# Kernel tuning notes

Hardware: AMD Instinct MI355X
Metric: run time of the kernel (lower is better)

Reference implementation:

```python
import jax, jax.numpy as jnp
import numpy as np

N_BASIS = 8
CUTOFF = 5.0
NORM_FACTOR = 16.0


def setup_inputs() -> dict:
    key = jax.random.key(0)
    ks = jax.random.split(key, 10)
    N, E, C = 20000, 320000, 32
    s = 1.0 / np.sqrt(C)
    return {
        "node0": jax.random.normal(ks[0], (N, C), jnp.float32),
        "node1": jax.random.normal(ks[1], (N, C, 3), jnp.float32),
        "node2": jax.random.normal(ks[2], (N, C, 3, 3), jnp.float32),
        "rij": jax.random.normal(ks[3], (E, 3), jnp.float32) * 1.5,
        "Wrad": jax.random.normal(ks[4], (11, N_BASIS, C), jnp.float32) * 0.3,
        "U": jax.random.normal(ks[5], (3, C, C), jnp.float32) * s,
        "V": jax.random.normal(ks[6], (8, C, C), jnp.float32) * s,
        "Wg": jax.random.normal(ks[7], (3, C, C), jnp.float32) * s,
        "idx_i": jax.random.randint(ks[8], (E,), 0, N),
        "idx_j": jax.random.randint(ks[9], (E,), 0, N),
    }


def reference(node0, node1, node2, rij, Wrad, U, V, Wg, idx_i, idx_j):
    N, C = node0.shape
    # radial basis (Gaussian RBF * cosine cutoff envelope)
    dist = jnp.sqrt(jnp.sum(rij * rij, -1) + 1e-12)           # [E]
    rhat = rij / dist[:, None]                                 # [E,3]
    centers = jnp.linspace(0.5, CUTOFF, N_BASIS, dtype=node0.dtype)
    fc = 0.5 * (jnp.cos(jnp.pi * jnp.clip(dist / CUTOFF, 0.0, 1.0)) + 1.0)
    rbf = jnp.exp(-4.0 * (dist[:, None] - centers) ** 2) * fc[:, None]  # [E,B]
    # per-coupling-path radial filters: 11 paths (in_way, r_way, out_way)
    w = jnp.einsum('eb,pbc->pec', rbf, Wrad)                   # [11,E,C]
    # gather neighbor (node_j) features per edge
    g0 = node0[idx_j]                                          # [E,C]
    g1 = node1[idx_j]                                          # [E,C,3]
    g2 = node2[idx_j]                                          # [E,C,3,3]
    m1 = rhat                                                  # [E,3]
    m2 = rhat[:, :, None] * rhat[:, None, :]                   # [E,3,3]
    # graph conv: contract node_j tensor with r-way moment, weighted by radial filter
    # paths: 0:(0,0,0) 1:(0,1,1) 2:(0,2,2) 3:(1,0,1) 4:(1,1,0) 5:(1,1,2)
    #        6:(1,2,1) 7:(2,0,2) 8:(2,1,1) 9:(2,2,0) 10:(2,2,2)
    msg0 = (g0 * w[0]
            + jnp.einsum('eca,ea->ec', g1, m1) * w[4]
            + jnp.einsum('ecab,eab->ec', g2, m2) * w[9])
    msg1 = (jnp.einsum('ec,ea->eca', g0 * w[1], m1)
            + g1 * w[3][:, :, None]
            + jnp.einsum('eca,eab->ecb', g1, m2) * w[6][:, :, None]
            + jnp.einsum('ecab,eb->eca', g2, m1) * w[8][:, :, None])
    msg2 = (jnp.einsum('ec,eab->ecab', g0 * w[2], m2)
            + jnp.einsum('eca,eb->ecab', g1 * w[5][:, :, None], m1)
            + g2 * w[7][:, :, None, None]
            + jnp.einsum('ecab,ebd->ecad', g2, m2) * w[10][:, :, None, None])
    # scatter_add aggregation into per-atom features, normalized
    a0 = jax.ops.segment_sum(msg0, idx_i, num_segments=N) / NORM_FACTOR
    a1 = jax.ops.segment_sum(msg1, idx_i, num_segments=N) / NORM_FACTOR
    a2 = jax.ops.segment_sum(msg2, idx_i, num_segments=N) / NORM_FACTOR
    # multi-body self-interaction (2-body linear U + 3-body products V)
    y0 = (jnp.einsum('nc,cd->nd', a0, U[0])
          + jnp.einsum('nc,cd->nd', a0 * a0, V[0])
          + jnp.einsum('nc,cd->nd', jnp.einsum('nca,nca->nc', a1, a1), V[3])
          + jnp.einsum('nc,cd->nd', jnp.einsum('ncab,ncab->nc', a2, a2), V[6]))
    y1 = (jnp.einsum('nca,cd->nda', a1, U[1])
          + jnp.einsum('nca,cd->nda', a0[:, :, None] * a1, V[1])
          + jnp.einsum('nca,cd->nda', jnp.einsum('nca,ncab->ncb', a1, a2), V[5]))
    y2 = (jnp.einsum('ncab,cd->ndab', a2, U[2])
          + jnp.einsum('ncab,cd->ndab', a0[:, :, None, None] * a2, V[2])
          + jnp.einsum('ncab,cd->ndab', a1[:, :, :, None] * a1[:, :, None, :], V[4])
          + jnp.einsum('ncab,cd->ndab', jnp.einsum('ncab,ncbd->ncad', a2, a2), V[7]))
    # gated nonlinearity (scalar channel gates tensor ways) + residual add
    new0 = node0 + jax.nn.silu(y0 @ Wg[0])
    new1 = node1 + y1 * jax.nn.silu(y0 @ Wg[1])[:, :, None]
    new2 = node2 + y2 * jax.nn.silu(y0 @ Wg[2])[:, :, None, None]
    return (new0, new1, new2)
```

## Files before the change

### kernel.cpp

```cpp
#include <hip/hip_runtime.h>
#include <hip/hip_fp16.h>

#define NCH 32
#define NB 8
#define NPB 8

typedef __attribute__((ext_vector_type(2))) _Float16 half2r;

__device__ __forceinline__ unsigned short f2h(float f) {
    return __half_as_ushort(__float2half_rn(f));
}
__device__ __forceinline__ float h2f_lo(unsigned int u) {
    half2r v = __builtin_bit_cast(half2r, u);
    return (float)v.x;
}
__device__ __forceinline__ float h2f_hi(unsigned int u) {
    half2r v = __builtin_bit_cast(half2r, u);
    return (float)v.y;
}
__device__ __forceinline__ unsigned int pack2h(float lo, float hi) {
    return (unsigned int)f2h(lo) | ((unsigned int)f2h(hi) << 16);
}

__device__ __forceinline__ float fdot2u(unsigned int a, unsigned int b, float c) {
#if __has_builtin(__builtin_amdgcn_fdot2)
    return __builtin_amdgcn_fdot2(__builtin_bit_cast(half2r, a),
                                  __builtin_bit_cast(half2r, b), c, false);
#else
    half2r av = __builtin_bit_cast(half2r, a);
    half2r bv = __builtin_bit_cast(half2r, b);
    return c + (float)av.x * (float)bv.x + (float)av.y * (float)bv.y;
#endif
}

__device__ __forceinline__ void acc8h(float& y, uint4 w, uint4 f) {
    y = fdot2u(w.x, f.x, y);
    y = fdot2u(w.y, f.y, y);
    y = fdot2u(w.z, f.z, y);
    y = fdot2u(w.w, f.w, y);
}
__device__ __forceinline__ void acc8fh(float& y, uint4 w, float4 a, float4 b) {
    y += h2f_lo(w.x) * a.x + h2f_hi(w.x) * a.y + h2f_lo(w.y) * a.z + h2f_hi(w.y) * a.w
       + h2f_lo(w.z) * b.x + h2f_hi(w.z) * b.y + h2f_lo(w.w) * b.z + h2f_hi(w.w) * b.w;
}

__global__ __launch_bounds__(256) void wprep_kernel(
    const float* __restrict__ U, const float* __restrict__ V,
    const float* __restrict__ Wg, unsigned short* __restrict__ wswz)
{
    int idx = blockIdx.x * 256 + threadIdx.x;
    if (idx >= 14 * 1024) return;
    int m = idx >> 10, r = idx & 1023;
    int c = r >> 5, d = r & 31;
    float v;
    if (m < 3)       v = U[m * 1024 + c * 32 + d];
    else if (m < 11) v = V[(m - 3) * 1024 + c * 32 + d];
    else             v = Wg[(m - 11) * 1024 + c * 32 + d];
    wswz[m * 1024 + (c >> 3) * 256 + d * 8 + (c & 7)] = f2h(v);
}

__global__ __launch_bounds__(256) void wprep_rad_kernel(
    const float* __restrict__ Wrad, unsigned int* __restrict__ wradp)
{
    int idx = blockIdx.x * 256 + threadIdx.x;
    if (idx >= 11 * 4 * 32) return;
    int c = idx & 31, bb = (idx >> 5) & 3, p = idx >> 7;
    float lo = Wrad[p * 256 + (2 * bb) * 32 + c] * (1.0f / 16.0f);
    float hi = Wrad[p * 256 + (2 * bb + 1) * 32 + c] * (1.0f / 16.0f);
    wradp[(p * 4 + bb) * 32 + c] = pack2h(lo, hi);
}

__global__ __launch_bounds__(256) void hist_kernel(
    const int* __restrict__ idx_i, int* __restrict__ counts, int E)
{
    int e = blockIdx.x * 256 + threadIdx.x;
    if (e < E) atomicAdd(&counts[idx_i[e]], 1);
}

__global__ __launch_bounds__(256) void scan_reduce_kernel(
    const int* __restrict__ counts, int* __restrict__ blocksums, int N)
{
    const int tid = threadIdx.x;
    const int base = blockIdx.x * 1024;
    int v = 0;
    #pragma unroll
    for (int k = 0; k < 4; ++k) {
        int i = base + tid * 4 + k;
        if (i < N) v += counts[i];
    }
    #pragma unroll
    for (int off = 1; off < 64; off <<= 1) v += __shfl_xor(v, off, 64);
    __shared__ int wsum[4];
    if ((tid & 63) == 0) wsum[tid >> 6] = v;
    __syncthreads();
    if (tid == 0) blocksums[blockIdx.x] = wsum[0] + wsum[1] + wsum[2] + wsum[3];
}

__global__ void scan_top_kernel(
    const int* __restrict__ blocksums, int* __restrict__ bases,
    int* __restrict__ offsets, int nb, int N)
{
    int l = threadIdx.x;
    int v = (l < nb) ? blocksums[l] : 0;
    int incl = v;
    #pragma unroll
    for (int off = 1; off < 64; off <<= 1) {
        int t = __shfl_up(incl, off, 64);
        if (l >= off) incl += t;
    }
    if (l < nb) bases[l] = incl - v;
    if (l == nb - 1) offsets[N] = incl;
}

__global__ __launch_bounds__(256) void scan_write_kernel(
    int* __restrict__ cursor, const int* __restrict__ bases,
    int* __restrict__ offsets, int N)
{
    const int tid = threadIdx.x;
    const int i0 = blockIdx.x * 1024 + tid * 4;
    int v[4]; int lsum = 0;
    #pragma unroll
    for (int k = 0; k < 4; ++k) {
        int i = i0 + k;
        v[k] = (i < N) ? cursor[i] : 0;
        lsum += v[k];
    }
    int incl = lsum;
    #pragma unroll
    for (int off = 1; off < 64; off <<= 1) {
        int t = __shfl_up(incl, off, 64);
        if ((tid & 63) >= off) incl += t;
    }
    __shared__ int wsum[4];
    if ((tid & 63) == 63) wsum[tid >> 6] = incl;
    __syncthreads();
    int add = bases[blockIdx.x];
    for (int w = 0; w < (tid >> 6); ++w) add += wsum[w];
    int run = add + incl - lsum;
    #pragma unroll
    for (int k = 0; k < 4; ++k) {
        int i = i0 + k;
        if (i < N) { offsets[i] = run; cursor[i] = run; run += v[k]; }
    }
}

__global__ __launch_bounds__(256) void scatter_meta_kernel(
    const int* __restrict__ idx_i, const int* __restrict__ idx_j,
    const float* __restrict__ rij, int* __restrict__ cursor,
    int* __restrict__ jord, float4* __restrict__ meta2, int E)
{
    int e = blockIdx.x * 256 + threadIdx.x;
    if (e >= E) return;
    float rx = rij[3 * e + 0], ry = rij[3 * e + 1], rz = rij[3 * e + 2];
    float dist = sqrtf(rx * rx + ry * ry + rz * rz + 1e-12f);
    float inv = 1.0f / dist;
    float tcl = fminf(dist * 0.2f, 1.0f);
    float fc = 0.5f * (cosf(3.14159265358979f * tcl) + 1.0f);
    float rbf[NB];
    #pragma unroll
    for (int b = 0; b < NB; ++b) {
        float dd = dist - (0.5f + (float)b * (4.5f / 7.0f));
        rbf[b] = expf(-4.0f * dd * dd) * fc;
    }
    unsigned int rb01 = pack2h(rbf[0], rbf[1]);
    unsigned int rb23 = pack2h(rbf[2], rbf[3]);
    unsigned int rb45 = pack2h(rbf[4], rbf[5]);
    unsigned int rb67 = pack2h(rbf[6], rbf[7]);
    int slot = atomicAdd(&cursor[idx_i[e]], 1);
    jord[slot] = idx_j[e];
    meta2[2 * slot + 0] = make_float4(rx * inv, ry * inv, rz * inv, __uint_as_float(rb01));
    meta2[2 * slot + 1] = make_float4(__uint_as_float(rb23), __uint_as_float(rb45),
                                      __uint_as_float(rb67), 0.0f);
}

__global__ __launch_bounds__(256) void transpose_nodes_kernel(
    const float* __restrict__ node0, const float* __restrict__ node1,
    const float* __restrict__ node2, uint4* __restrict__ ncomb, int N)
{
    int n = blockIdx.x * 8 + (threadIdx.x >> 5);
    int c = threadIdx.x & 31;
    if (n >= N) return;
    float G0 = node0[n * 32 + c];
    float G1[3];
    #pragma unroll
    for (int a = 0; a < 3; ++a) G1[a] = node1[n * 96 + c * 3 + a];
    float G2[9];
    #pragma unroll
    for (int k = 0; k < 9; ++k) G2[k] = node2[n * 288 + c * 9 + k];
    uint4 P0, P1;
    P0.x = pack2h(G0,    G1[0]);
    P0.y = pack2h(G1[1], G1[2]);
    P0.z = pack2h(G2[0], G2[1]);
    P0.w = pack2h(G2[2], G2[3]);
    P1.x = pack2h(G2[4], G2[5]);
    P1.y = pack2h(G2[6], G2[7]);
    P1.z = pack2h(G2[8], 0.0f);
    P1.w = 0u;
    ncomb[(size_t)n * 64 + c]      = P0;
    ncomb[(size_t)n * 64 + 32 + c] = P1;
}

__global__ __launch_bounds__(256) void aggregate_kernel(
    const uint4* __restrict__ ncomb, const unsigned int* __restrict__ wradp,
    const int* __restrict__ jord, const float4* __restrict__ meta2,
    const int* __restrict__ offsets,
    float* __restrict__ a0, float* __restrict__ a1, float* __restrict__ a2,
    int N)
{
    const int lane = threadIdx.x & 63;
    const int c = lane & 31;
    const int side = lane >> 5;
    const int n = blockIdx.x * 4 + (threadIdx.x >> 6);
    if (n >= N) return;

    unsigned int wr[11][4];
    #pragma unroll
    for (int p = 0; p < 11; ++p)
        #pragma unroll
        for (int bb = 0; bb < 4; ++bb)
            wr[p][bb] = wradp[(p * 4 + bb) * 32 + c];

    const int beg = offsets[n], end = offsets[n + 1];
    const int nit = (end - beg + 1) >> 1;

    float A0 = 0.f;
    float A1[3] = {0.f, 0.f, 0.f};
    float A2[9] = {0.f, 0.f, 0.f, 0.f, 0.f, 0.f, 0.f, 0.f, 0.f};

    int e = beg + side;
    bool vn = (e < end);
    int jn = 0;
    if (vn) jn = jord[e];
    bool vn2 = (e + 2 < end);
    int jn2 = 0;
    if (vn2) jn2 = jord[e + 2];

    uint4 P0n = {0, 0, 0, 0}, P1n = {0, 0, 0, 0};
    float4 M0n = make_float4(0.f, 0.f, 0.f, 0.f), M1n = M0n;
    if (vn) {
        const uint4* src = ncomb + ((size_t)jn << 6) + c;
        P0n = src[0];
        P1n = src[32];
        M0n = meta2[2 * e + 0];
        M1n = meta2[2 * e + 1];
    }

    for (int it = 0; it < nit; ++it) {
        const uint4 P0 = P0n, P1 = P1n;
        const float4 M0 = M0n, M1 = M1n;
        const bool v = vn;

        const int en = e + 2;
        vn = vn2;
        jn = jn2;
        if (vn) {
            const uint4* src = ncomb + ((size_t)jn << 6) + c;
            P0n = src[0];
            P1n = src[32];
            M0n = meta2[2 * en + 0];
            M1n = meta2[2 * en + 1];
        }
        vn2 = (en + 2 < end);
        if (vn2) jn2 = jord[en + 2];
        e = en;

        if (v) {
            const float h0 = M0.x, h1 = M0.y, h2 = M0.z;
            const unsigned int rb01 = __float_as_uint(M0.w);
            const unsigned int rb23 = __float_as_uint(M1.x);
            const unsigned int rb45 = __float_as_uint(M1.y);
            const unsigned int rb67 = __float_as_uint(M1.z);

            float w[11];
            #pragma unroll
            for (int p = 0; p < 11; ++p)
                w[p] = fdot2u(rb01, wr[p][0],
                       fdot2u(rb23, wr[p][1],
                       fdot2u(rb45, wr[p][2],
                       fdot2u(rb67, wr[p][3], 0.0f))));

            const float G0   = h2f_lo(P0.x);
            float G1[3];
            G1[0] = h2f_hi(P0.x); G1[1] = h2f_lo(P0.y); G1[2] = h2f_hi(P0.y);
            float G2[9];
            G2[0] = h2f_lo(P0.z); G2[1] = h2f_hi(P0.z);
            G2[2] = h2f_lo(P0.w); G2[3] = h2f_hi(P0.w);
            G2[4] = h2f_lo(P1.x); G2[5] = h2f_hi(P1.x);
            G2[6] = h2f_lo(P1.y); G2[7] = h2f_hi(P1.y);
            G2[8] = h2f_lo(P1.z);

            const float hh[3] = {h0, h1, h2};
            const float s1 = G1[0] * h0 + G1[1] * h1 + G1[2] * h2;
            float tt[3];
            #pragma unroll
            for (int a = 0; a < 3; ++a)
                tt[a] = G2[a * 3 + 0] * h0 + G2[a * 3 + 1] * h1 + G2[a * 3 + 2] * h2;
            const float s2 = tt[0] * h0 + tt[1] * h1 + tt[2] * h2;

            A0 += G0 * w[0] + s1 * w[4] + s2 * w[9];
            #pragma unroll
            for (int a = 0; a < 3; ++a)
                A1[a] += (G0 * w[1] + s1 * w[6]) * hh[a] + G1[a] * w[3] + tt[a] * w[8];
            #pragma unroll
            for (int a = 0; a < 3; ++a) {
                float pre = G0 * w[2] * hh[a] + G1[a] * w[5] + tt[a] * w[10];
                #pragma unroll
                for (int b = 0; b < 3; ++b)
                    A2[a * 3 + b] += pre * hh[b] + G2[a * 3 + b] * w[7];
            }
        }
    }

    A0 += __shfl_xor(A0, 32, 64);
    #pragma unroll
    for (int a = 0; a < 3; ++a) A1[a] += __shfl_xor(A1[a], 32, 64);
    #pragma unroll
    for (int k = 0; k < 9; ++k) A2[k] += __shfl_xor(A2[k], 32, 64);

    if (side == 0) {
        a0[n * 32 + c] = A0;
        #pragma unroll
        for (int a = 0; a < 3; ++a) a1[n * 96 + a * 32 + c] = A1[a];
        #pragma unroll
        for (int k = 0; k < 9; ++k) a2[n * 288 + k * 32 + c] = A2[k];
    }
}

__global__ __launch_bounds__(256) void node_kernel(
    const float* __restrict__ node0, const float* __restrict__ node1,
    const float* __restrict__ node2, const unsigned short* __restrict__ wswz,
    float* __restrict__ out0, float* __restrict__ out1, float* __restrict__ out2,
    int N)
{
    __shared__ alignas(16) unsigned short wT[14 * 1024];
    __shared__ alignas(16) unsigned short feat[NPB * 49 * 32];
    __shared__ alignas(16) float y0s[NPB][32];

    {
        const uint4* src = reinterpret_cast<const uint4*>(wswz);
        uint4* dst = reinterpret_cast<uint4*>(wT);
        for (int i = threadIdx.x; i < 14 * 128; i += 256) dst[i] = src[i];
    }

    const int g = threadIdx.x >> 5;
    const int lane = threadIdx.x & 31;
    const int n = blockIdx.x * NPB + g;
    const bool active = (n < N);

    if (active) {
        const int c = lane;
        float A0 = out0[n * 32 + c];
        float A1[3], A2[9];
        #pragma unroll
        for (int a = 0; a < 3; ++a) A1[a] = out1[n * 96 + a * 32 + c];
        #pragma unroll
        for (int k = 0; k < 9; ++k) A2[k] = out2[n * 288 + k * 32 + c];

        unsigned short* F = &feat[g * 49 * 32];
        F[0 * 32 + c] = f2h(A0);
        F[1 * 32 + c] = f2h(A0 * A0);
        F[2 * 32 + c] = f2h(A1[0] * A1[0] + A1[1] * A1[1] + A1[2] * A1[2]);
        float n2 = 0.f;
        #pragma unroll
        for (int k = 0; k < 9; ++k) n2 += A2[k] * A2[k];
        F[3 * 32 + c] = f2h(n2);
        #pragma unroll
        for (int a = 0; a < 3; ++a) {
            F[(4 + a) * 32 + c] = f2h(A1[a]);
            F[(7 + a) * 32 + c] = f2h(A0 * A1[a]);
        }
        #pragma unroll
        for (int b = 0; b < 3; ++b) {
            float s = A1[0] * A2[0 * 3 + b] + A1[1] * A2[1 * 3 + b] + A1[2] * A2[2 * 3 + b];
            F[(10 + b) * 32 + c] = f2h(s);
        }
        #pragma unroll
        for (int k = 0; k < 9; ++k) {
            F[(13 + k) * 32 + c] = f2h(A2[k]);
            F[(22 + k) * 32 + c] = f2h(A0 * A2[k]);
        }
        #pragma unroll
        for (int a = 0; a < 3; ++a)
            #pragma unroll
            for (int b = 0; b < 3; ++b)
                F[(31 + a * 3 + b) * 32 + c] = f2h(A1[a] * A1[b]);
        #pragma unroll
        for (int a = 0; a < 3; ++a)
            #pragma unroll
            for (int dd = 0; dd < 3; ++dd) {
                float s = A2[a * 3 + 0] * A2[0 * 3 + dd] + A2[a * 3 + 1] * A2[1 * 3 + dd]
                        + A2[a * 3 + 2] * A2[2 * 3 + dd];
                F[(40 + a * 3 + dd) * 32 + c] = f2h(s);
            }
    }
    __syncthreads();

    const int d = lane;
    float y0v = 0.f;
    float y1v[3] = {0.f, 0.f, 0.f};
    float y2v[9] = {0.f, 0.f, 0.f, 0.f, 0.f, 0.f, 0.f, 0.f, 0.f};

    if (active) {
        const uint4* W4 = reinterpret_cast<const uint4*>(wT);
        const uint4* F4 = reinterpret_cast<const uint4*>(&feat[g * 49 * 32]);
        for (int q = 0; q < 4; ++q) {
            const int q32d = q * 32 + d;
            acc8h(y0v, W4[0 * 128 + q32d], F4[0 * 4 + q]);
            acc8h(y0v, W4[3 * 128 + q32d], F4[1 * 4 + q]);
            acc8h(y0v, W4[6 * 128 + q32d], F4[2 * 4 + q]);
            acc8h(y0v, W4[9 * 128 + q32d], F4[3 * 4 + q]);
            uint4 wU1 = W4[1 * 128 + q32d];
            uint4 wV1 = W4[4 * 128 + q32d];
            uint4 wV5 = W4[8 * 128 + q32d];
            #pragma unroll
            for (int a = 0; a < 3; ++a) {
                acc8h(y1v[a], wU1, F4[(4 + a) * 4 + q]);
                acc8h(y1v[a], wV1, F4[(7 + a) * 4 + q]);
                acc8h(y1v[a], wV5, F4[(10 + a) * 4 + q]);
            }
            uint4 wU2 = W4[2 * 128 + q32d];
            uint4 wV2 = W4[5 * 128 + q32d];
            uint4 wV4 = W4[7 * 128 + q32d];
            uint4 wV7 = W4[10 * 128 + q32d];
            #pragma unroll
            for (int k = 0; k < 9; ++k) {
                acc8h(y2v[k], wU2, F4[(13 + k) * 4 + q]);
                acc8h(y2v[k], wV2, F4[(22 + k) * 4 + q]);
                acc8h(y2v[k], wV4, F4[(31 + k) * 4 + q]);
                acc8h(y2v[k], wV7, F4[(40 + k) * 4 + q]);
            }
        }
        y0s[g][d] = y0v;
    }
    __syncthreads();

    if (!active) return;

    float t0 = 0.f, t1 = 0.f, t2 = 0.f;
    {
        const uint4* W4 = reinterpret_cast<const uint4*>(wT);
        const float4* Y4 = reinterpret_cast<const float4*>(y0s[g]);
        #pragma unroll
        for (int q = 0; q < 4; ++q) {
            const int q32d = q * 32 + d;
            float4 ya = Y4[2 * q], yb = Y4[2 * q + 1];
            acc8fh(t0, W4[11 * 128 + q32d], ya, yb);
            acc8fh(t1, W4[12 * 128 + q32d], ya, yb);
            acc8fh(t2, W4[13 * 128 + q32d], ya, yb);
        }
    }
    float s0 = t0 / (1.0f + expf(-t0));
    float s1 = t1 / (1.0f + expf(-t1));
    float s2 = t2 / (1.0f + expf(-t2));

    out0[n * 32 + d] = node0[n * 32 + d] + s0;
    #pragma unroll
    for (int a = 0; a < 3; ++a)
        out1[n * 96 + d * 3 + a] = node1[n * 96 + d * 3 + a] + y1v[a] * s1;
    #pragma unroll
    for (int k = 0; k < 9; ++k)
        out2[n * 288 + d * 9 + k] = node2[n * 288 + d * 9 + k] + y2v[k] * s2;
}

extern "C" void kernel_launch(void* const* d_in, const int* in_sizes, int n_in,
                              void* d_out, int out_size, void* d_ws, size_t ws_size,
                              hipStream_t stream)
{
    const float* node0 = (const float*)d_in[0];
    const float* node1 = (const float*)d_in[1];
    const float* node2 = (const float*)d_in[2];
    const float* rij   = (const float*)d_in[3];
    const float* Wrad  = (const float*)d_in[4];
    const float* U     = (const float*)d_in[5];
    const float* V     = (const float*)d_in[6];
    const float* Wg    = (const float*)d_in[7];
    const int* idx_i   = (const int*)d_in[8];
    const int* idx_j   = (const int*)d_in[9];

    const int N = in_sizes[0] / 32;
    const int E = in_sizes[3] / 3;

    float* out0 = (float*)d_out;
    float* out1 = out0 + (size_t)N * 32;
    float* out2 = out1 + (size_t)N * 96;

    size_t off = 0;
    auto walloc = [&](size_t bytes) -> void* {
        off = (off + 63) & ~(size_t)63;
        void* p = (char*)d_ws + off;
        off += bytes;
        return p;
    };
    int*    cursor    = (int*)   walloc((size_t)N * 4);
    int*    offsets   = (int*)   walloc((size_t)(N + 1) * 4);
    int*    blocksums = (int*)   walloc(64 * 4);
    int*    bases     = (int*)   walloc(64 * 4);
    int*    jord      = (int*)   walloc((size_t)E * 4);
    float4* meta2     = (float4*)walloc((size_t)E * 2 * sizeof(float4));
    uint4*  ncomb     = (uint4*) walloc((size_t)N * 64 * sizeof(uint4));
    unsigned short* wswz = (unsigned short*)walloc(14 * 1024 * 2);
    unsigned int*  wradp = (unsigned int*)walloc(11 * 4 * 32 * 4);
    (void)ws_size;

    const int nb = (N + 1023) / 1024;

    hipMemsetAsync(cursor, 0, (size_t)N * sizeof(int), stream);

    wprep_kernel<<<dim3(56), dim3(256), 0, stream>>>(U, V, Wg, wswz);
    wprep_rad_kernel<<<dim3(6), dim3(256), 0, stream>>>(Wrad, wradp);
    hist_kernel<<<dim3((E + 255) / 256), dim3(256), 0, stream>>>(idx_i, cursor, E);
    scan_reduce_kernel<<<dim3(nb), dim3(256), 0, stream>>>(cursor, blocksums, N);
    scan_top_kernel<<<dim3(1), dim3(64), 0, stream>>>(blocksums, bases, offsets, nb, N);
    scan_write_kernel<<<dim3(nb), dim3(256), 0, stream>>>(cursor, bases, offsets, N);
    scatter_meta_kernel<<<dim3((E + 255) / 256), dim3(256), 0, stream>>>(
        idx_i, idx_j, rij, cursor, jord, meta2, E);
    transpose_nodes_kernel<<<dim3((N + 7) / 8), dim3(256), 0, stream>>>(
        node0, node1, node2, ncomb, N);

    aggregate_kernel<<<dim3((N + 3) / 4), dim3(256), 0, stream>>>(
        ncomb, wradp, jord, meta2, offsets, out0, out1, out2, N);

    node_kernel<<<dim3((N + NPB - 1) / NPB), dim3(256), 0, stream>>>(
        node0, node1, node2, wswz, out0, out1, out2, N);
}
```

Baseline: 274.6 us.

## Split packed node table into compact arrays and deepen aggregate gather pipeline

The padded 64-byte-per-channel fp16 node table is replaced by three tightly packed arrays (8, 16 and 2 bytes per channel), so each gathered edge reads 26 bytes per channel instead of 32. The transpose kernel now stages node1/node2 through shared memory so its global reads are coalesced. The aggregate loop keeps two edges in flight per half-wave with clamped prefetch, which removes the branchy validity tracking. The radial weights are also re-laid out so each channel loads them as uint4 vectors. In exchange, each edge issues three separate gathers instead of two, and the clamped prefetch makes redundant loads at the tail of every node's edge list.

```diff
diff --git a/kernel.cpp b/kernel.cpp
--- a/kernel.cpp
+++ b/kernel.cpp
@@ -67,7 +67,7 @@
     int c = idx & 31, bb = (idx >> 5) & 3, p = idx >> 7;
     float lo = Wrad[p * 256 + (2 * bb) * 32 + c] * (1.0f / 16.0f);
     float hi = Wrad[p * 256 + (2 * bb + 1) * 32 + c] * (1.0f / 16.0f);
-    wradp[(p * 4 + bb) * 32 + c] = pack2h(lo, hi);
+    wradp[c * 44 + p * 4 + bb] = pack2h(lo, hi);
 }
 
 __global__ __launch_bounds__(256) void hist_kernel(
@@ -175,33 +175,109 @@
 
 __global__ __launch_bounds__(256) void transpose_nodes_kernel(
     const float* __restrict__ node0, const float* __restrict__ node1,
-    const float* __restrict__ node2, uint4* __restrict__ ncomb, int N)
-{
-    int n = blockIdx.x * 8 + (threadIdx.x >> 5);
-    int c = threadIdx.x & 31;
+    const float* __restrict__ node2, uint2* __restrict__ t0g,
+    uint4* __restrict__ t1g, unsigned short* __restrict__ t2g, int N)
+{
+    __shared__ float s1[8 * 96];
+    __shared__ float s2[8 * 288];
+    const int nb0 = blockIdx.x * 8;
+    const int remN = N - nb0;
+    if (remN >= 8) {
+        const float4* src1 = reinterpret_cast<const float4*>(node1 + (size_t)nb0 * 96);
+        float4* d1 = reinterpret_cast<float4*>(s1);
+        for (int i = threadIdx.x; i < 192; i += 256) d1[i] = src1[i];
+        const float4* src2 = reinterpret_cast<const float4*>(node2 + (size_t)nb0 * 288);
+        float4* d2 = reinterpret_cast<float4*>(s2);
+        for (int i = threadIdx.x; i < 576; i += 256) d2[i] = src2[i];
+    } else {
+        const int tot1 = remN * 96;
+        for (int i = threadIdx.x; i < 768; i += 256)
+            s1[i] = (i < tot1) ? node1[(size_t)nb0 * 96 + i] : 0.f;
+        const int tot2 = remN * 288;
+        for (int i = threadIdx.x; i < 2304; i += 256)
+            s2[i] = (i < tot2) ? node2[(size_t)nb0 * 288 + i] : 0.f;
+    }
+    __syncthreads();
+
+    const int g = threadIdx.x >> 5;
+    const int c = threadIdx.x & 31;
+    const int n = nb0 + g;
     if (n >= N) return;
-    float G0 = node0[n * 32 + c];
+
+    float G0 = node0[(size_t)n * 32 + c];
     float G1[3];
     #pragma unroll
-    for (int a = 0; a < 3; ++a) G1[a] = node1[n * 96 + c * 3 + a];
+    for (int a = 0; a < 3; ++a) G1[a] = s1[g * 96 + c * 3 + a];
     float G2[9];
     #pragma unroll
-    for (int k = 0; k < 9; ++k) G2[k] = node2[n * 288 + c * 9 + k];
-    uint4 P0, P1;
-    P0.x = pack2h(G0,    G1[0]);
+    for (int k = 0; k < 9; ++k) G2[k] = s2[g * 288 + c * 9 + k];
+
+    const size_t b = ((size_t)n << 5) + c;
+    uint2 P0;
+    P0.x = pack2h(G0, G1[0]);
     P0.y = pack2h(G1[1], G1[2]);
-    P0.z = pack2h(G2[0], G2[1]);
-    P0.w = pack2h(G2[2], G2[3]);
-    P1.x = pack2h(G2[4], G2[5]);
-    P1.y = pack2h(G2[6], G2[7]);
-    P1.z = pack2h(G2[8], 0.0f);
-    P1.w = 0u;
-    ncomb[(size_t)n * 64 + c]      = P0;
-    ncomb[(size_t)n * 64 + 32 + c] = P1;
+    uint4 P1;
+    P1.x = pack2h(G2[0], G2[1]);
+    P1.y = pack2h(G2[2], G2[3]);
+    P1.z = pack2h(G2[4], G2[5]);
+    P1.w = pack2h(G2[6], G2[7]);
+    t0g[b] = P0;
+    t1g[b] = P1;
+    t2g[b] = f2h(G2[8]);
+}
+
+__device__ __forceinline__ void edge_compute(
+    uint2 P0, uint4 P1, unsigned short g28, float4 M0, float4 M1,
+    const uint4 wrq[11], float& A0, float (&A1)[3], float (&A2)[9])
+{
+    const float h0 = M0.x, h1 = M0.y, h2 = M0.z;
+    const unsigned int rb01 = __float_as_uint(M0.w);
+    const unsigned int rb23 = __float_as_uint(M1.x);
+    const unsigned int rb45 = __float_as_uint(M1.y);
+    const unsigned int rb67 = __float_as_uint(M1.z);
+
+    float w[11];
+    #pragma unroll
+    for (int p = 0; p < 11; ++p)
+        w[p] = fdot2u(rb01, wrq[p].x,
+               fdot2u(rb23, wrq[p].y,
+               fdot2u(rb45, wrq[p].z,
+               fdot2u(rb67, wrq[p].w, 0.0f))));
+
+    const float G0 = h2f_lo(P0.x);
+    float G1[3];
+    G1[0] = h2f_hi(P0.x); G1[1] = h2f_lo(P0.y); G1[2] = h2f_hi(P0.y);
+    float G2[9];
+    G2[0] = h2f_lo(P1.x); G2[1] = h2f_hi(P1.x);
+    G2[2] = h2f_lo(P1.y); G2[3] = h2f_hi(P1.y);
+    G2[4] = h2f_lo(P1.z); G2[5] = h2f_hi(P1.z);
+    G2[6] = h2f_lo(P1.w); G2[7] = h2f_hi(P1.w);
+    G2[8] = __half2float(__ushort_as_half(g28));
+
+    const float hh[3] = {h0, h1, h2};
+    const float s1 = G1[0] * h0 + G1[1] * h1 + G1[2] * h2;
+    float tt[3];
+    #pragma unroll
+    for (int a = 0; a < 3; ++a)
+        tt[a] = G2[a * 3 + 0] * h0 + G2[a * 3 + 1] * h1 + G2[a * 3 + 2] * h2;
+    const float s2 = tt[0] * h0 + tt[1] * h1 + tt[2] * h2;
+
+    A0 += G0 * w[0] + s1 * w[4] + s2 * w[9];
+    #pragma unroll
+    for (int a = 0; a < 3; ++a)
+        A1[a] += (G0 * w[1] + s1 * w[6]) * hh[a] + G1[a] * w[3] + tt[a] * w[8];
+    #pragma unroll
+    for (int a = 0; a < 3; ++a) {
+        float pre = G0 * w[2] * hh[a] + G1[a] * w[5] + tt[a] * w[10];
+        #pragma unroll
+        for (int b = 0; b < 3; ++b)
+            A2[a * 3 + b] += pre * hh[b] + G2[a * 3 + b] * w[7];
+    }
 }
 
 __global__ __launch_bounds__(256) void aggregate_kernel(
-    const uint4* __restrict__ ncomb, const unsigned int* __restrict__ wradp,
+    const uint2* __restrict__ t0g, const uint4* __restrict__ t1g,
+    const unsigned short* __restrict__ t2g, const unsigned int* __restrict__ wradp,
     const int* __restrict__ jord, const float4* __restrict__ meta2,
     const int* __restrict__ offsets,
     float* __restrict__ a0, float* __restrict__ a1, float* __restrict__ a2,
@@ -213,102 +289,69 @@
     const int n = blockIdx.x * 4 + (threadIdx.x >> 6);
     if (n >= N) return;
 
-    unsigned int wr[11][4];
-    #pragma unroll
-    for (int p = 0; p < 11; ++p)
-        #pragma unroll
-        for (int bb = 0; bb < 4; ++bb)
-            wr[p][bb] = wradp[(p * 4 + bb) * 32 + c];
+    uint4 wrq[11];
+    {
+        const uint4* wrv = reinterpret_cast<const uint4*>(wradp) + c * 11;
+        #pragma unroll
+        for (int p = 0; p < 11; ++p) wrq[p] = wrv[p];
+    }
 
     const int beg = offsets[n], end = offsets[n + 1];
-    const int nit = (end - beg + 1) >> 1;
+    const int deg = end - beg;
 
     float A0 = 0.f;
     float A1[3] = {0.f, 0.f, 0.f};
     float A2[9] = {0.f, 0.f, 0.f, 0.f, 0.f, 0.f, 0.f, 0.f, 0.f};
 
-    int e = beg + side;
-    bool vn = (e < end);
-    int jn = 0;
-    if (vn) jn = jord[e];
-    bool vn2 = (e + 2 < end);
-    int jn2 = 0;
-    if (vn2) jn2 = jord[e + 2];
-
-    uint4 P0n = {0, 0, 0, 0}, P1n = {0, 0, 0, 0};
-    float4 M0n = make_float4(0.f, 0.f, 0.f, 0.f), M1n = M0n;
-    if (vn) {
-        const uint4* src = ncomb + ((size_t)jn << 6) + c;
-        P0n = src[0];
-        P1n = src[32];
-        M0n = meta2[2 * e + 0];
-        M1n = meta2[2 * e + 1];
-    }
-
-    for (int it = 0; it < nit; ++it) {
-        const uint4 P0 = P0n, P1 = P1n;
-        const float4 M0 = M0n, M1 = M1n;
-        const bool v = vn;
-
-        const int en = e + 2;
-        vn = vn2;
-        jn = jn2;
-        if (vn) {
-            const uint4* src = ncomb + ((size_t)jn << 6) + c;
-            P0n = src[0];
-            P1n = src[32];
-            M0n = meta2[2 * en + 0];
-            M1n = meta2[2 * en + 1];
-        }
-        vn2 = (en + 2 < end);
-        if (vn2) jn2 = jord[en + 2];
-        e = en;
-
-        if (v) {
-            const float h0 = M0.x, h1 = M0.y, h2 = M0.z;
-            const unsigned int rb01 = __float_as_uint(M0.w);
-            const unsigned int rb23 = __float_as_uint(M1.x);
-            const unsigned int rb45 = __float_as_uint(M1.y);
-            const unsigned int rb67 = __float_as_uint(M1.z);
-
-            float w[11];
-            #pragma unroll
-            for (int p = 0; p < 11; ++p)
-                w[p] = fdot2u(rb01, wr[p][0],
-                       fdot2u(rb23, wr[p][1],
-                       fdot2u(rb45, wr[p][2],
-                       fdot2u(rb67, wr[p][3], 0.0f))));
-
-            const float G0   = h2f_lo(P0.x);
-            float G1[3];
-            G1[0] = h2f_hi(P0.x); G1[1] = h2f_lo(P0.y); G1[2] = h2f_hi(P0.y);
-            float G2[9];
-            G2[0] = h2f_lo(P0.z); G2[1] = h2f_hi(P0.z);
-            G2[2] = h2f_lo(P0.w); G2[3] = h2f_hi(P0.w);
-            G2[4] = h2f_lo(P1.x); G2[5] = h2f_hi(P1.x);
-            G2[6] = h2f_lo(P1.y); G2[7] = h2f_hi(P1.y);
-            G2[8] = h2f_lo(P1.z);
-
-            const float hh[3] = {h0, h1, h2};
-            const float s1 = G1[0] * h0 + G1[1] * h1 + G1[2] * h2;
-            float tt[3];
-            #pragma unroll
-            for (int a = 0; a < 3; ++a)
-                tt[a] = G2[a * 3 + 0] * h0 + G2[a * 3 + 1] * h1 + G2[a * 3 + 2] * h2;
-            const float s2 = tt[0] * h0 + tt[1] * h1 + tt[2] * h2;
-
-            A0 += G0 * w[0] + s1 * w[4] + s2 * w[9];
-            #pragma unroll
-            for (int a = 0; a < 3; ++a)
-                A1[a] += (G0 * w[1] + s1 * w[6]) * hh[a] + G1[a] * w[3] + tt[a] * w[8];
-            #pragma unroll
-            for (int a = 0; a < 3; ++a) {
-                float pre = G0 * w[2] * hh[a] + G1[a] * w[5] + tt[a] * w[10];
-                #pragma unroll
-                for (int b = 0; b < 3; ++b)
-                    A2[a * 3 + b] += pre * hh[b] + G2[a * 3 + b] * w[7];
-            }
-        }
+    if (deg > 0) {
+        const int last = end - 1;
+        int eA = beg + side;
+        int eB = eA + 2;
+        int jA2 = jord[min(eA + 4, last)];
+        int jB2 = jord[min(eB + 4, last)];
+
+        uint2 P0A, P0B; uint4 P1A, P1B; unsigned short s2A, s2B;
+        float4 M0A, M1A, M0B, M1B;
+        {
+            const int jA = jord[min(eA, last)];
+            const size_t b = ((size_t)jA << 5) + c;
+            P0A = t0g[b]; P1A = t1g[b]; s2A = t2g[b];
+            const int em = min(eA, last);
+            M0A = meta2[2 * em]; M1A = meta2[2 * em + 1];
+        }
+        {
+            const int jB = jord[min(eB, last)];
+            const size_t b = ((size_t)jB << 5) + c;
+            P0B = t0g[b]; P1B = t1g[b]; s2B = t2g[b];
+            const int em = min(eB, last);
+            M0B = meta2[2 * em]; M1B = meta2[2 * em + 1];
+        }
+
+        const int M = (deg + 3) >> 2;
+
+#define SLOT_STEP(P0s, P1s, s2s, M0s, M1s, eS, jS2)                         \
+        {                                                                   \
+            const uint2 P0 = P0s; const uint4 P1 = P1s;                     \
+            const unsigned short g28 = s2s;                                 \
+            const float4 Mm0 = M0s, Mm1 = M1s;                              \
+            const bool v = (eS < end);                                      \
+            const int eSn = eS + 4;                                         \
+            {                                                               \
+                const size_t b = ((size_t)jS2 << 5) + c;                    \
+                P0s = t0g[b]; P1s = t1g[b]; s2s = t2g[b];                   \
+                const int em = min(eSn, last);                              \
+                M0s = meta2[2 * em]; M1s = meta2[2 * em + 1];               \
+            }                                                               \
+            jS2 = jord[min(eSn + 4, last)];                                 \
+            if (v) edge_compute(P0, P1, g28, Mm0, Mm1, wrq, A0, A1, A2);    \
+            eS = eSn;                                                       \
+        }
+
+        for (int m = 0; m < M; ++m) {
+            SLOT_STEP(P0A, P1A, s2A, M0A, M1A, eA, jA2)
+            SLOT_STEP(P0B, P1B, s2B, M0B, M1B, eB, jB2)
+        }
+#undef SLOT_STEP
     }
 
     A0 += __shfl_xor(A0, 32, 64);
@@ -497,7 +540,9 @@
     int*    bases     = (int*)   walloc(64 * 4);
     int*    jord      = (int*)   walloc((size_t)E * 4);
     float4* meta2     = (float4*)walloc((size_t)E * 2 * sizeof(float4));
-    uint4*  ncomb     = (uint4*) walloc((size_t)N * 64 * sizeof(uint4));
+    uint2*  t0g       = (uint2*) walloc((size_t)N * 32 * sizeof(uint2));
+    uint4*  t1g       = (uint4*) walloc((size_t)N * 32 * sizeof(uint4));
+    unsigned short* t2g = (unsigned short*)walloc((size_t)N * 32 * 2);
     unsigned short* wswz = (unsigned short*)walloc(14 * 1024 * 2);
     unsigned int*  wradp = (unsigned int*)walloc(11 * 4 * 32 * 4);
     (void)ws_size;
@@ -515,10 +560,10 @@
     scatter_meta_kernel<<<dim3((E + 255) / 256), dim3(256), 0, stream>>>(
         idx_i, idx_j, rij, cursor, jord, meta2, E);
     transpose_nodes_kernel<<<dim3((N + 7) / 8), dim3(256), 0, stream>>>(
-        node0, node1, node2, ncomb, N);
+        node0, node1, node2, t0g, t1g, t2g, N);
 
     aggregate_kernel<<<dim3((N + 3) / 4), dim3(256), 0, stream>>>(
-        ncomb, wradp, jord, meta2, offsets, out0, out1, out2, N);
+        t0g, t1g, t2g, wradp, jord, meta2, offsets, out0, out1, out2, N);
 
     node_kernel<<<dim3((N + NPB - 1) / NPB), dim3(256), 0, stream>>>(
         node0, node1, node2, wswz, out0, out1, out2, N);
```

Result: no change. 271.6 us (-1.1%).
